# Kernel tuning notes

Measured on AMD Instinct MI355X. Metric: run time of the kernel, lower is better.

## Reference

```python
import jax, jax.numpy as jnp
import numpy as np

NEG_SLOPE = 0.2

def gat_conv(x, src, dst, W, att_src, att_dst, bias, heads, out_c, concat):
    # x: [N, F_in]; src/dst: [E] (self-loops already included)
    N = x.shape[0]
    xh = (x @ W).reshape(N, heads, out_c)               # [N,H,C]
    a_src = jnp.sum(xh * att_src, axis=-1)              # [N,H]
    a_dst = jnp.sum(xh * att_dst, axis=-1)              # [N,H]
    alpha = a_src[src] + a_dst[dst]                     # [E,H]
    alpha = jax.nn.leaky_relu(alpha, NEG_SLOPE)
    # segment softmax over destination node
    m = jax.ops.segment_max(alpha, dst, num_segments=N) # [N,H]
    e = jnp.exp(alpha - m[dst])                         # [E,H]
    s = jax.ops.segment_sum(e, dst, num_segments=N)     # [N,H]
    coef = e / s[dst]                                   # [E,H]
    msg = xh[src] * coef[:, :, None]                    # [E,H,C]
    out = jax.ops.segment_sum(msg, dst, num_segments=N) # [N,H,C]
    if concat:
        out = out.reshape(N, heads * out_c)
    else:
        out = out.mean(axis=1)
    return out + bias

def setup_inputs() -> dict:
    key = jax.random.key(0)
    ks = jax.random.split(key, 12)
    N, E = 50000, 400000
    Fin, Hc, H, Fout = 128, 16, 8, 128
    x = jax.random.normal(ks[0], (N, Fin), dtype=jnp.float32)
    src = jax.random.randint(ks[1], (E,), 0, N, dtype=jnp.int32)
    dst = jax.random.randint(ks[2], (E,), 0, N, dtype=jnp.int32)
    g = lambda k, shp, fan: (jax.random.normal(k, shp, dtype=jnp.float32) * (1.0 / np.sqrt(fan))).astype(jnp.float32)
    return {
        'x': x, 'src': src, 'dst': dst,
        'W1': g(ks[3], (Fin, H * Hc), Fin),
        'att_src1': g(ks[4], (H, Hc), Hc),
        'att_dst1': g(ks[5], (H, Hc), Hc),
        'b1': jnp.zeros((H * Hc,), dtype=jnp.float32),
        'W2': g(ks[6], (H * Hc, Fout), H * Hc),
        'att_src2': g(ks[7], (1, Fout), Fout),
        'att_dst2': g(ks[8], (1, Fout), Fout),
        'b2': jnp.zeros((Fout,), dtype=jnp.float32),
    }

def reference(x, src, dst, W1, att_src1, att_dst1, b1, W2, att_src2, att_dst2, b2):
    N = x.shape[0]
    loops = jnp.arange(N, dtype=src.dtype)
    s = jnp.concatenate([src, loops])  # add_self_loops=True (PyG default)
    d = jnp.concatenate([dst, loops])
    h = gat_conv(x, s, d, W1, att_src1, att_dst1, b1, heads=8, out_c=16, concat=True)
    h = jax.nn.elu(h)
    out = gat_conv(h, s, d, W2, att_src2, att_dst2, b2, heads=1, out_c=128, concat=False)
    return out
```

## Files before the change

### kernel.cpp

```cpp
#include <hip/hip_runtime.h>
#include <hip/hip_bf16.h>
#include <math.h>

#define NEG_SLOPE 0.2f
#define SCAN_BLOCK 256
#define BK 32

__global__ __launch_bounds__(256) void zero_int_kernel(int* __restrict__ p, int n) {
    int i = blockIdx.x * 256 + threadIdx.x;
    if (i < n) p[i] = 0;
}

__global__ __launch_bounds__(256) void count_deg_kernel(const int* __restrict__ dst,
                                                        int E, int N, int* __restrict__ deg) {
    int e = blockIdx.x * 256 + threadIdx.x;
    int Etot = E + N;
    if (e >= Etot) return;
    int d = (e < E) ? dst[e] : (e - E);
    atomicAdd(&deg[d], 1);
}

__global__ __launch_bounds__(SCAN_BLOCK) void deg_partial_kernel(const int* __restrict__ deg,
                                                                 int* __restrict__ part, int N) {
    __shared__ int red[SCAN_BLOCK];
    int t = threadIdx.x;
    int i = blockIdx.x * SCAN_BLOCK + t;
    red[t] = (i < N) ? deg[i] : 0;
    __syncthreads();
    #pragma unroll
    for (int off = SCAN_BLOCK / 2; off > 0; off >>= 1) {
        if (t < off) red[t] += red[t + off];
        __syncthreads();
    }
    if (t == 0) part[blockIdx.x] = red[0];
}

__global__ __launch_bounds__(1024) void scan_part_kernel(int* __restrict__ part, int nPart) {
    __shared__ int s[1024];
    int t = threadIdx.x;
    int v = (t < nPart) ? part[t] : 0;
    s[t] = v;
    __syncthreads();
    for (int off = 1; off < 1024; off <<= 1) {
        int u = (t >= off) ? s[t - off] : 0;
        __syncthreads();
        s[t] += u;
        __syncthreads();
    }
    if (t < nPart) part[t] = (t == 0) ? 0 : s[t - 1];
}

__global__ __launch_bounds__(SCAN_BLOCK) void scan_final_kernel(const int* __restrict__ deg,
                                                                const int* __restrict__ part,
                                                                int* __restrict__ row_ptr, int N) {
    __shared__ int s[SCAN_BLOCK];
    int t = threadIdx.x;
    int i = blockIdx.x * SCAN_BLOCK + t;
    int v = (i < N) ? deg[i] : 0;
    s[t] = v;
    __syncthreads();
    #pragma unroll
    for (int off = 1; off < SCAN_BLOCK; off <<= 1) {
        int u = (t >= off) ? s[t - off] : 0;
        __syncthreads();
        s[t] += u;
        __syncthreads();
    }
    int incl = s[t];
    int base = part[blockIdx.x];
    if (i < N) row_ptr[i] = base + incl - v;
    if (i == N - 1) row_ptr[N] = base + incl;
}

__global__ __launch_bounds__(256) void scatter_kernel(const int* __restrict__ src,
                                                      const int* __restrict__ dst,
                                                      int E, int N,
                                                      const int* __restrict__ row_ptr,
                                                      int* __restrict__ cursor,
                                                      int* __restrict__ col_src) {
    int e = blockIdx.x * 256 + threadIdx.x;
    int Etot = E + N;
    if (e >= Etot) return;
    int d, s;
    if (e < E) { d = dst[e]; s = src[e]; } else { d = e - E; s = e - E; }
    int pos = atomicAdd(&cursor[d], 1);
    col_src[row_ptr[d] + pos] = s;
}

__global__ __launch_bounds__(128) void gemm_rb_kernel(const float* __restrict__ X,
                                                      const float* __restrict__ W,
                                                      float* __restrict__ Y, int N) {
    __shared__ float Xs[BK][68];
    __shared__ float Wt[BK][128];
    const int t = threadIdx.x;
    const int r0 = blockIdx.x * 64;
    const int lane = t & 63, w = t >> 6;
    const int lx = lane & 15, ly = lane >> 4;
    const int row_base = w * 32 + ly * 8;
    const int c1 = lx * 4, c2 = 64 + lx * 4;

    float acc[8][8];
    #pragma unroll
    for (int i = 0; i < 8; ++i)
        #pragma unroll
        for (int j = 0; j < 8; ++j) acc[i][j] = 0.f;

    for (int kt = 0; kt < 128; kt += BK) {
        __syncthreads();
        #pragma unroll
        for (int i = 0; i < 4; ++i) {
            int idx = i * 128 + t;
            int row = idx >> 3, k4 = idx & 7;
            int gr = r0 + row;
            float4 g = make_float4(0.f, 0.f, 0.f, 0.f);
            if (gr < N) g = *(const float4*)(X + (size_t)gr * 128 + kt + k4 * 4);
            Xs[k4 * 4 + 0][row] = g.x;
            Xs[k4 * 4 + 1][row] = g.y;
            Xs[k4 * 4 + 2][row] = g.z;
            Xs[k4 * 4 + 3][row] = g.w;
        }
        #pragma unroll
        for (int i = 0; i < 8; ++i) {
            int idx = i * 128 + t;
            int wr = idx >> 5, c4 = idx & 31;
            *(float4*)&Wt[wr][c4 * 4] = *(const float4*)(W + (size_t)(kt + wr) * 128 + c4 * 4);
        }
        __syncthreads();

        #pragma unroll 8
        for (int k = 0; k < BK; ++k) {
            float4 a0 = *(const float4*)&Xs[k][row_base];
            float4 a1 = *(const float4*)&Xs[k][row_base + 4];
            float4 b0 = *(const float4*)&Wt[k][c1];
            float4 b1 = *(const float4*)&Wt[k][c2];
            float a[8] = {a0.x, a0.y, a0.z, a0.w, a1.x, a1.y, a1.z, a1.w};
            float b[8] = {b0.x, b0.y, b0.z, b0.w, b1.x, b1.y, b1.z, b1.w};
            #pragma unroll
            for (int i = 0; i < 8; ++i)
                #pragma unroll
                for (int j = 0; j < 8; ++j)
                    acc[i][j] = fmaf(a[i], b[j], acc[i][j]);
        }
    }

    #pragma unroll
    for (int i = 0; i < 8; ++i) {
        int gr = r0 + row_base + i;
        if (gr < N) {
            *(float4*)(Y + (size_t)gr * 128 + c1) =
                make_float4(acc[i][0], acc[i][1], acc[i][2], acc[i][3]);
            *(float4*)(Y + (size_t)gr * 128 + c2) =
                make_float4(acc[i][4], acc[i][5], acc[i][6], acc[i][7]);
        }
    }
}

__global__ __launch_bounds__(256) void attdot1_kernel(const float* __restrict__ xh,
                                                      const float* __restrict__ attS,
                                                      const float* __restrict__ attD,
                                                      float* __restrict__ asrc,
                                                      float* __restrict__ adst, int N) {
    int node = blockIdx.x * 4 + (threadIdx.x >> 6);
    int lane = threadIdx.x & 63;
    if (node >= N) return;
    const float* row = xh + (size_t)node * 128;
    float x1 = row[lane], x2 = row[lane + 64];
    float s1 = x1 * attS[lane], s2 = x2 * attS[lane + 64];
    float d1 = x1 * attD[lane], d2 = x2 * attD[lane + 64];
    #pragma unroll
    for (int off = 8; off >= 1; off >>= 1) {
        s1 += __shfl_xor(s1, off, 64);
        s2 += __shfl_xor(s2, off, 64);
        d1 += __shfl_xor(d1, off, 64);
        d2 += __shfl_xor(d2, off, 64);
    }
    if ((lane & 15) == 0) {
        int h = lane >> 4;
        asrc[node * 8 + h]     = s1;
        asrc[node * 8 + h + 4] = s2;
        adst[node * 8 + h]     = d1;
        adst[node * 8 + h + 4] = d2;
    }
}

__global__ __launch_bounds__(256) void attdot2_kernel(const float* __restrict__ xh,
                                                      const float* __restrict__ attS,
                                                      const float* __restrict__ attD,
                                                      float* __restrict__ asrc,
                                                      float* __restrict__ adst, int N) {
    int node = blockIdx.x * 4 + (threadIdx.x >> 6);
    int lane = threadIdx.x & 63;
    if (node >= N) return;
    const float* row = xh + (size_t)node * 128;
    float x1 = row[lane], x2 = row[lane + 64];
    float ts = x1 * attS[lane] + x2 * attS[lane + 64];
    float td = x1 * attD[lane] + x2 * attD[lane + 64];
    #pragma unroll
    for (int off = 32; off >= 1; off >>= 1) {
        ts += __shfl_xor(ts, off, 64);
        td += __shfl_xor(td, off, 64);
    }
    if (lane == 0) { asrc[node] = ts; adst[node] = td; }
}

__global__ __launch_bounds__(256) void agg1_kernel(const float* __restrict__ xh,
                                                   const float* __restrict__ asrc,
                                                   const float* __restrict__ adst,
                                                   const int* __restrict__ row_ptr,
                                                   const int* __restrict__ col_src,
                                                   const float* __restrict__ b1,
                                                   float* __restrict__ out, int N) {
    int node = blockIdx.x * 4 + (threadIdx.x >> 6);
    int lane = threadIdx.x & 63;
    if (node >= N) return;
    int h1 = lane >> 4;
    float ad1 = adst[node * 8 + h1];
    float ad2 = adst[node * 8 + h1 + 4];
    int beg = row_ptr[node], end = row_ptr[node + 1];
    float m1 = -INFINITY, m2 = -INFINITY;
    float s1 = 0.f, s2 = 0.f, a1 = 0.f, a2 = 0.f;
    for (int e = beg; e < end; ++e) {
        int sv = col_src[e];
        float e1 = asrc[sv * 8 + h1] + ad1;
        float e2 = asrc[sv * 8 + h1 + 4] + ad2;
        e1 = (e1 > 0.f) ? e1 : NEG_SLOPE * e1;
        e2 = (e2 > 0.f) ? e2 : NEG_SLOPE * e2;
        float x1 = xh[(size_t)sv * 128 + lane];
        float x2 = xh[(size_t)sv * 128 + lane + 64];
        if (e1 > m1) { float r = __expf(m1 - e1); s1 *= r; a1 *= r; m1 = e1; }
        float p1 = __expf(e1 - m1);
        s1 += p1; a1 = fmaf(p1, x1, a1);
        if (e2 > m2) { float r = __expf(m2 - e2); s2 *= r; a2 *= r; m2 = e2; }
        float p2 = __expf(e2 - m2);
        s2 += p2; a2 = fmaf(p2, x2, a2);
    }
    float o1 = a1 / s1 + b1[lane];
    float o2 = a2 / s2 + b1[lane + 64];
    o1 = (o1 > 0.f) ? o1 : (__expf(o1) - 1.f);
    o2 = (o2 > 0.f) ? o2 : (__expf(o2) - 1.f);
    out[(size_t)node * 128 + lane]      = o1;
    out[(size_t)node * 128 + lane + 64] = o2;
}

__global__ __launch_bounds__(256) void agg2_kernel(const float* __restrict__ xh,
                                                   const float* __restrict__ asrc,
                                                   const float* __restrict__ adst,
                                                   const int* __restrict__ row_ptr,
                                                   const int* __restrict__ col_src,
                                                   const float* __restrict__ b2,
                                                   float* __restrict__ out, int N) {
    int node = blockIdx.x * 4 + (threadIdx.x >> 6);
    int lane = threadIdx.x & 63;
    if (node >= N) return;
    float ad = adst[node];
    int beg = row_ptr[node], end = row_ptr[node + 1];
    float m = -INFINITY, s = 0.f, a1 = 0.f, a2 = 0.f;
    for (int e = beg; e < end; ++e) {
        int sv = col_src[e];
        float al = asrc[sv] + ad;
        al = (al > 0.f) ? al : NEG_SLOPE * al;
        float x1 = xh[(size_t)sv * 128 + lane];
        float x2 = xh[(size_t)sv * 128 + lane + 64];
        if (al > m) { float r = __expf(m - al); s *= r; a1 *= r; a2 *= r; m = al; }
        float p = __expf(al - m);
        s += p;
        a1 = fmaf(p, x1, a1);
        a2 = fmaf(p, x2, a2);
    }
    out[(size_t)node * 128 + lane]      = a1 / s + b2[lane];
    out[(size_t)node * 128 + lane + 64] = a2 / s + b2[lane + 64];
}

extern "C" void kernel_launch(void* const* d_in, const int* in_sizes, int n_in,
                              void* d_out, int out_size, void* d_ws, size_t ws_size,
                              hipStream_t stream) {
    const float* x        = (const float*)d_in[0];
    const int*   src      = (const int*)d_in[1];
    const int*   dst      = (const int*)d_in[2];
    const float* W1       = (const float*)d_in[3];
    const float* att_src1 = (const float*)d_in[4];
    const float* att_dst1 = (const float*)d_in[5];
    const float* b1       = (const float*)d_in[6];
    const float* W2       = (const float*)d_in[7];
    const float* att_src2 = (const float*)d_in[8];
    const float* att_dst2 = (const float*)d_in[9];
    const float* b2       = (const float*)d_in[10];

    const int N = in_sizes[0] / 128;
    const int E = in_sizes[1];
    const int Etot = E + N;

    float* fws   = (float*)d_ws;
    float* xh    = fws;
    float* asrc1 = xh + (size_t)N * 128;
    float* adst1 = asrc1 + (size_t)N * 8;
    float* asrc2 = adst1 + (size_t)N * 8;
    float* adst2 = asrc2 + N;
    int*   deg     = (int*)(adst2 + N);
    int*   cursor  = deg + N;
    int*   row_ptr = cursor + N;
    int*   col_src = row_ptr + N + 1;
    int*   part    = col_src + Etot;

    float* h = (float*)d_out;

    const int nodeBlocks = (N + 3) / 4;
    const int edgeBlocks = (Etot + 255) / 256;
    const int gemmBlocks = (N + 63) / 64;
    const int scanBlocks = (N + SCAN_BLOCK - 1) / SCAN_BLOCK;

    zero_int_kernel<<<(2 * N + 255) / 256, 256, 0, stream>>>(deg, 2 * N);
    count_deg_kernel<<<edgeBlocks, 256, 0, stream>>>(dst, E, N, deg);
    deg_partial_kernel<<<scanBlocks, SCAN_BLOCK, 0, stream>>>(deg, part, N);
    scan_part_kernel<<<1, 1024, 0, stream>>>(part, scanBlocks);
    scan_final_kernel<<<scanBlocks, SCAN_BLOCK, 0, stream>>>(deg, part, row_ptr, N);
    scatter_kernel<<<edgeBlocks, 256, 0, stream>>>(src, dst, E, N, row_ptr, cursor, col_src);

    gemm_rb_kernel<<<gemmBlocks, 128, 0, stream>>>(x, W1, xh, N);
    attdot1_kernel<<<nodeBlocks, 256, 0, stream>>>(xh, att_src1, att_dst1, asrc1, adst1, N);
    agg1_kernel<<<nodeBlocks, 256, 0, stream>>>(xh, asrc1, adst1, row_ptr, col_src, b1, h, N);

    gemm_rb_kernel<<<gemmBlocks, 128, 0, stream>>>(h, W2, xh, N);
    attdot2_kernel<<<nodeBlocks, 256, 0, stream>>>(xh, att_src2, att_dst2, asrc2, adst2, N);
    agg2_kernel<<<nodeBlocks, 256, 0, stream>>>(xh, asrc2, adst2, row_ptr, col_src, b2, (float*)d_out, N);
}
```

Measured before the change: 340.9 us.

## Gather bf16-packed features in aggregation and use two-pass softmax

The GEMM epilogue now also writes a bf16 copy of the projected features, packing columns c and c+64 into one 32-bit word. Both aggregation kernels gather this packed copy, which halves the bytes read per neighbor row. The online softmax with its rescaling branches is replaced by a first pass that computes the max logit, followed by exp2-based accumulation. This costs an extra bf16 write in the GEMM, a second pass over the neighbor logits, and bf16 rounding error in the aggregated features.

```diff
diff --git a/kernel.cpp b/kernel.cpp
--- a/kernel.cpp
+++ b/kernel.cpp
@@ -5,6 +5,15 @@
 #define NEG_SLOPE 0.2f
 #define SCAN_BLOCK 256
 #define BK 32
+#define LOG2E 1.4426950408889634f
+
+__device__ __forceinline__ unsigned pack_bf16_pair(float lo, float hi) {
+    unsigned ul = __float_as_uint(lo);
+    ul += 0x7fffu + ((ul >> 16) & 1u);
+    unsigned uh = __float_as_uint(hi);
+    uh += 0x7fffu + ((uh >> 16) & 1u);
+    return (ul >> 16) | (uh & 0xffff0000u);
+}
 
 __global__ __launch_bounds__(256) void zero_int_kernel(int* __restrict__ p, int n) {
     int i = blockIdx.x * 256 + threadIdx.x;
@@ -89,7 +98,8 @@
 
 __global__ __launch_bounds__(128) void gemm_rb_kernel(const float* __restrict__ X,
                                                       const float* __restrict__ W,
-                                                      float* __restrict__ Y, int N) {
+                                                      float* __restrict__ Y,
+                                                      unsigned* __restrict__ Ybf, int N) {
     __shared__ float Xs[BK][68];
     __shared__ float Wt[BK][128];
     const int t = threadIdx.x;
@@ -151,6 +161,12 @@
                 make_float4(acc[i][0], acc[i][1], acc[i][2], acc[i][3]);
             *(float4*)(Y + (size_t)gr * 128 + c2) =
                 make_float4(acc[i][4], acc[i][5], acc[i][6], acc[i][7]);
+            uint4 pk;
+            pk.x = pack_bf16_pair(acc[i][0], acc[i][4]);
+            pk.y = pack_bf16_pair(acc[i][1], acc[i][5]);
+            pk.z = pack_bf16_pair(acc[i][2], acc[i][6]);
+            pk.w = pack_bf16_pair(acc[i][3], acc[i][7]);
+            *(uint4*)(Ybf + (size_t)gr * 64 + c1) = pk;
         }
     }
 }
@@ -203,7 +219,7 @@
     if (lane == 0) { asrc[node] = ts; adst[node] = td; }
 }
 
-__global__ __launch_bounds__(256) void agg1_kernel(const float* __restrict__ xh,
+__global__ __launch_bounds__(256) void agg1_kernel(const unsigned* __restrict__ xhp,
                                                    const float* __restrict__ asrc,
                                                    const float* __restrict__ adst,
                                                    const int* __restrict__ row_ptr,
@@ -217,21 +233,32 @@
     float ad1 = adst[node * 8 + h1];
     float ad2 = adst[node * 8 + h1 + 4];
     int beg = row_ptr[node], end = row_ptr[node + 1];
-    float m1 = -INFINITY, m2 = -INFINITY;
+
+    float m1 = -1e30f, m2 = -1e30f;
+    for (int e = beg; e < end; ++e) {
+        int sv = col_src[e];
+        float e1 = asrc[sv * 8 + h1] + ad1;
+        float e2 = asrc[sv * 8 + h1 + 4] + ad2;
+        e1 = fmaxf(e1, NEG_SLOPE * e1);
+        e2 = fmaxf(e2, NEG_SLOPE * e2);
+        m1 = fmaxf(m1, e1);
+        m2 = fmaxf(m2, e2);
+    }
+    m1 *= LOG2E; m2 *= LOG2E;
+
     float s1 = 0.f, s2 = 0.f, a1 = 0.f, a2 = 0.f;
     for (int e = beg; e < end; ++e) {
         int sv = col_src[e];
         float e1 = asrc[sv * 8 + h1] + ad1;
         float e2 = asrc[sv * 8 + h1 + 4] + ad2;
-        e1 = (e1 > 0.f) ? e1 : NEG_SLOPE * e1;
-        e2 = (e2 > 0.f) ? e2 : NEG_SLOPE * e2;
-        float x1 = xh[(size_t)sv * 128 + lane];
-        float x2 = xh[(size_t)sv * 128 + lane + 64];
-        if (e1 > m1) { float r = __expf(m1 - e1); s1 *= r; a1 *= r; m1 = e1; }
-        float p1 = __expf(e1 - m1);
+        e1 = fmaxf(e1, NEG_SLOPE * e1);
+        e2 = fmaxf(e2, NEG_SLOPE * e2);
+        float p1 = exp2f(fmaf(e1, LOG2E, -m1));
+        float p2 = exp2f(fmaf(e2, LOG2E, -m2));
+        unsigned v = xhp[(size_t)sv * 64 + lane];
+        float x1 = __uint_as_float(v << 16);
+        float x2 = __uint_as_float(v & 0xffff0000u);
         s1 += p1; a1 = fmaf(p1, x1, a1);
-        if (e2 > m2) { float r = __expf(m2 - e2); s2 *= r; a2 *= r; m2 = e2; }
-        float p2 = __expf(e2 - m2);
         s2 += p2; a2 = fmaf(p2, x2, a2);
     }
     float o1 = a1 / s1 + b1[lane];
@@ -242,7 +269,7 @@
     out[(size_t)node * 128 + lane + 64] = o2;
 }
 
-__global__ __launch_bounds__(256) void agg2_kernel(const float* __restrict__ xh,
+__global__ __launch_bounds__(256) void agg2_kernel(const unsigned* __restrict__ xhp,
                                                    const float* __restrict__ asrc,
                                                    const float* __restrict__ adst,
                                                    const int* __restrict__ row_ptr,
@@ -254,15 +281,24 @@
     if (node >= N) return;
     float ad = adst[node];
     int beg = row_ptr[node], end = row_ptr[node + 1];
-    float m = -INFINITY, s = 0.f, a1 = 0.f, a2 = 0.f;
+
+    float m = -1e30f;
+    for (int e = beg; e < end; ++e) {
+        float al = asrc[col_src[e]] + ad;
+        al = fmaxf(al, NEG_SLOPE * al);
+        m = fmaxf(m, al);
+    }
+    m *= LOG2E;
+
+    float s = 0.f, a1 = 0.f, a2 = 0.f;
     for (int e = beg; e < end; ++e) {
         int sv = col_src[e];
         float al = asrc[sv] + ad;
-        al = (al > 0.f) ? al : NEG_SLOPE * al;
-        float x1 = xh[(size_t)sv * 128 + lane];
-        float x2 = xh[(size_t)sv * 128 + lane + 64];
-        if (al > m) { float r = __expf(m - al); s *= r; a1 *= r; a2 *= r; m = al; }
-        float p = __expf(al - m);
+        al = fmaxf(al, NEG_SLOPE * al);
+        float p = exp2f(fmaf(al, LOG2E, -m));
+        unsigned v = xhp[(size_t)sv * 64 + lane];
+        float x1 = __uint_as_float(v << 16);
+        float x2 = __uint_as_float(v & 0xffff0000u);
         s += p;
         a1 = fmaf(p, x1, a1);
         a2 = fmaf(p, x2, a2);
@@ -301,6 +337,7 @@
     int*   row_ptr = cursor + N;
     int*   col_src = row_ptr + N + 1;
     int*   part    = col_src + Etot;
+    unsigned* xhp  = (unsigned*)(part + 1024);
 
     float* h = (float*)d_out;
 
@@ -316,11 +353,11 @@
     scan_final_kernel<<<scanBlocks, SCAN_BLOCK, 0, stream>>>(deg, part, row_ptr, N);
     scatter_kernel<<<edgeBlocks, 256, 0, stream>>>(src, dst, E, N, row_ptr, cursor, col_src);
 
-    gemm_rb_kernel<<<gemmBlocks, 128, 0, stream>>>(x, W1, xh, N);
+    gemm_rb_kernel<<<gemmBlocks, 128, 0, stream>>>(x, W1, xh, xhp, N);
     attdot1_kernel<<<nodeBlocks, 256, 0, stream>>>(xh, att_src1, att_dst1, asrc1, adst1, N);
-    agg1_kernel<<<nodeBlocks, 256, 0, stream>>>(xh, asrc1, adst1, row_ptr, col_src, b1, h, N);
-
-    gemm_rb_kernel<<<gemmBlocks, 128, 0, stream>>>(h, W2, xh, N);
+    agg1_kernel<<<nodeBlocks, 256, 0, stream>>>(xhp, asrc1, adst1, row_ptr, col_src, b1, h, N);
+
+    gemm_rb_kernel<<<gemmBlocks, 128, 0, stream>>>(h, W2, xh, xhp, N);
     attdot2_kernel<<<nodeBlocks, 256, 0, stream>>>(xh, att_src2, att_dst2, asrc2, adst2, N);
-    agg2_kernel<<<nodeBlocks, 256, 0, stream>>>(xh, asrc2, adst2, row_ptr, col_src, b2, (float*)d_out, N);
-}
+    agg2_kernel<<<nodeBlocks, 256, 0, stream>>>(xhp, asrc2, adst2, row_ptr, col_src, b2, (float*)d_out, N);
+}
```

Measured after the change: 404.8 us. 1.19x slower.
